# Kernel tuning notes

Measured on AMD Instinct MI355X. Metric: run time of the kernel, lower is better.

The kernel has to match this reference:

```python
import jax, jax.numpy as jnp
import numpy as np

N_USER = 100000
N_ITEM = 100000
E = 800000
IN_USER, IN_ITEM, HID, OUT = 256, 128, 128, 64


def _gconv(x_src, W, b, src, dst, n_src, n_dst):
    """DGL GraphConv, norm='both', transform-before-aggregate (in>=out here)."""
    ones = jnp.ones(src.shape[0], x_src.dtype)
    deg_out = jax.ops.segment_sum(ones, src, num_segments=n_src)
    deg_in = jax.ops.segment_sum(ones, dst, num_segments=n_dst)
    inv_out = jnp.maximum(deg_out, 1.0) ** -0.5
    inv_in = jnp.maximum(deg_in, 1.0) ** -0.5
    x = (x_src @ W) * inv_out[:, None]            # [n_src, out]
    agg = jax.ops.segment_sum(x[src], dst, num_segments=n_dst)  # scatter-add over edges
    return agg * inv_in[:, None] + b


def setup_inputs() -> dict:
    key = jax.random.key(0)
    ks = jax.random.split(key, 24)
    d = {
        "feat_user": jax.random.normal(ks[0], (N_USER, IN_USER), jnp.float32),
        "feat_item": jax.random.normal(ks[1], (N_ITEM, IN_ITEM), jnp.float32),
        "rates_src": jax.random.randint(ks[2], (E,), 0, N_USER, jnp.int32),
        "rates_dst": jax.random.randint(ks[3], (E,), 0, N_ITEM, jnp.int32),
        "rated_src": jax.random.randint(ks[4], (E,), 0, N_ITEM, jnp.int32),
        "rated_dst": jax.random.randint(ks[5], (E,), 0, N_USER, jnp.int32),
        "fol_src": jax.random.randint(ks[6], (E,), 0, N_USER, jnp.int32),
        "fol_dst": jax.random.randint(ks[7], (E,), 0, N_USER, jnp.int32),
    }
    def glorot(k, shp):
        lim = np.sqrt(6.0 / (shp[0] + shp[1]))
        return jax.random.uniform(k, shp, jnp.float32, -lim, lim)
    d["W1_rates"] = glorot(ks[8], (IN_USER, HID)); d["b1_rates"] = jnp.zeros((HID,), jnp.float32)
    d["W1_rated"] = glorot(ks[9], (IN_ITEM, HID)); d["b1_rated"] = jnp.zeros((HID,), jnp.float32)
    d["W1_fol"] = glorot(ks[10], (IN_USER, HID)); d["b1_fol"] = jnp.zeros((HID,), jnp.float32)
    d["W2_rates"] = glorot(ks[11], (HID, OUT)); d["b2_rates"] = jnp.zeros((OUT,), jnp.float32)
    d["W2_rated"] = glorot(ks[12], (HID, OUT)); d["b2_rated"] = jnp.zeros((OUT,), jnp.float32)
    d["W2_fol"] = glorot(ks[13], (HID, OUT)); d["b2_fol"] = jnp.zeros((OUT,), jnp.float32)
    return d


def reference(feat_user, feat_item, rates_src, rates_dst, rated_src, rated_dst,
              fol_src, fol_dst, W1_rates, b1_rates, W1_rated, b1_rated,
              W1_fol, b1_fol, W2_rates, b2_rates, W2_rated, b2_rated,
              W2_fol, b2_fol):
    # layer 1 (HeteroGraphConv, sum-aggregate across relations per dst ntype)
    h_item = _gconv(feat_user, W1_rates, b1_rates, rates_src, rates_dst, N_USER, N_ITEM)
    h_user = (_gconv(feat_item, W1_rated, b1_rated, rated_src, rated_dst, N_ITEM, N_USER)
              + _gconv(feat_user, W1_fol, b1_fol, fol_src, fol_dst, N_USER, N_USER))
    # relu (dropout = identity in eval mode)
    h_user = jax.nn.relu(h_user)
    h_item = jax.nn.relu(h_item)
    # layer 2
    o_item = _gconv(h_user, W2_rates, b2_rates, rates_src, rates_dst, N_USER, N_ITEM)
    o_user = (_gconv(h_item, W2_rated, b2_rated, rated_src, rated_dst, N_ITEM, N_USER)
              + _gconv(h_user, W2_fol, b2_fol, fol_src, fol_dst, N_USER, N_USER))
    return jnp.stack([o_user, o_item])  # [2, N, OUT]
```

## Files before the change

### kernel.cpp

```cpp
#include <hip/hip_runtime.h>
#include <math.h>

#define IN_USER 256
#define IN_ITEM 128
#define HID 128
#define OUTF 64
#define NRANGE 8
#define NCHUNK 16
#define MAXRB 12544

typedef unsigned short u16;
typedef unsigned int u32;
typedef __attribute__((ext_vector_type(8))) __bf16 bf16x8;
typedef __attribute__((ext_vector_type(4))) float f32x4;

__device__ __forceinline__ u16 f2bf(float f) {
    union { float f; u32 u; } c; c.f = f;
    return (u16)((c.u + 0x7fffu + ((c.u >> 16) & 1u)) >> 16);
}
__device__ __forceinline__ u32 pack2(float a, float b) {
    return (u32)f2bf(a) | ((u32)f2bf(b) << 16);
}

__global__ __launch_bounds__(512) void hist_ranges(
        const int* __restrict__ a0, int e0, const int* __restrict__ a1, int e1,
        const int* __restrict__ a2, int e2, const int* __restrict__ a3, int e3,
        const int* __restrict__ a4, int e4, const int* __restrict__ a5, int e5,
        int* __restrict__ hist, int NP, int RB) {
    __shared__ int h[MAXRB];
    const int a = blockIdx.z;
    const int* arr; int E;
    switch (a) {
        case 0: arr = a0; E = e0; break;
        case 1: arr = a1; E = e1; break;
        case 2: arr = a2; E = e2; break;
        case 3: arr = a3; E = e3; break;
        case 4: arr = a4; E = e4; break;
        default: arr = a5; E = e5; break;
    }
    const int c = blockIdx.y;
    const int lo = blockIdx.x * RB;
    const u32 rbu = (u32)RB;
    const int tid = threadIdx.x;
    for (int i = tid; i < RB; i += 512) h[i] = 0;
    __syncthreads();
    const int ec = (((E + NCHUNK - 1) / NCHUNK) + 3) & ~3;
    const int s0 = c * ec;
    const int s1 = (s0 + ec) < E ? (s0 + ec) : E;
    if (s1 > s0) {
        const int n4 = (s1 - s0) >> 2;
        const int4* p4 = reinterpret_cast<const int4*>(arr + s0);
        for (int i = tid; i < n4; i += 512) {
            const int4 A = p4[i];
            u32 ux = (u32)(A.x - lo); if (ux < rbu) atomicAdd(&h[ux], 1);
            u32 uy = (u32)(A.y - lo); if (uy < rbu) atomicAdd(&h[uy], 1);
            u32 uz = (u32)(A.z - lo); if (uz < rbu) atomicAdd(&h[uz], 1);
            u32 uw = (u32)(A.w - lo); if (uw < rbu) atomicAdd(&h[uw], 1);
        }
        for (int j = s0 + (n4 << 2) + tid; j < s1; j += 512) {
            const u32 u = (u32)(arr[j] - lo);
            if (u < rbu) atomicAdd(&h[u], 1);
        }
    }
    __syncthreads();
    int* out = hist + ((size_t)a * NCHUNK + c) * NP + lo;
    for (int i = tid; i < RB; i += 512) out[i] = h[i];
}

__global__ __launch_bounds__(256) void hist_reduce(
        int* __restrict__ hist, int* __restrict__ deg,
        float* __restrict__ inv, int NP) {
    const int a = blockIdx.y;
    const int v = blockIdx.x * 256 + threadIdx.x;
    if (v >= NP) return;
    int* h = hist + (size_t)a * NCHUNK * NP + v;
    int s = 0;
#pragma unroll
    for (int c = 0; c < NCHUNK; ++c) {
        const int t = h[(size_t)c * NP];
        if (a & 1) h[(size_t)c * NP] = s;
        s += t;
    }
    deg[(size_t)a * NP + v] = s;
    inv[(size_t)a * NP + v] = 1.0f / sqrtf((float)(s > 1 ? s : 1));
}

__global__ __launch_bounds__(256) void scan_part(
        const int* __restrict__ d0, const int* __restrict__ d1,
        const int* __restrict__ d2, int n0, int n1, int n2,
        int* __restrict__ partial, int nblk) {
    const int rel = blockIdx.y;
    const int* deg = rel == 0 ? d0 : (rel == 1 ? d1 : d2);
    const int n = rel == 0 ? n0 : (rel == 1 ? n1 : n2);
    const int base = blockIdx.x * 1024 + threadIdx.x * 4;
    int s = 0;
#pragma unroll
    for (int i = 0; i < 4; ++i) {
        const int idx = base + i;
        if (idx < n) s += deg[idx];
    }
    __shared__ int red[256];
    red[threadIdx.x] = s;
    __syncthreads();
#pragma unroll
    for (int off = 128; off > 0; off >>= 1) {
        if (threadIdx.x < off) red[threadIdx.x] += red[threadIdx.x + off];
        __syncthreads();
    }
    if (threadIdx.x == 0) partial[rel * nblk + blockIdx.x] = red[0];
}

__global__ __launch_bounds__(128) void scan_mid(int* __restrict__ partial, int nblk) {
    __shared__ int sc[128];
    const int rel = blockIdx.x;
    const int t = threadIdx.x;
    const int v = (t < nblk) ? partial[rel * nblk + t] : 0;
    sc[t] = v;
    __syncthreads();
    for (int off = 1; off < 128; off <<= 1) {
        const int u = (t >= off) ? sc[t - off] : 0;
        __syncthreads();
        sc[t] += u;
        __syncthreads();
    }
    if (t < nblk) partial[rel * nblk + t] = sc[t] - v;
}

__global__ __launch_bounds__(256) void scan_final(
        const int* __restrict__ d0, const int* __restrict__ d1,
        const int* __restrict__ d2, int n0, int n1, int n2,
        const int* __restrict__ partial,
        int* __restrict__ c0, int* __restrict__ c1, int* __restrict__ c2,
        int nblk) {
    const int rel = blockIdx.y;
    const int* deg = rel == 0 ? d0 : (rel == 1 ? d1 : d2);
    int* cur = rel == 0 ? c0 : (rel == 1 ? c1 : c2);
    const int n = rel == 0 ? n0 : (rel == 1 ? n1 : n2);
    const int base = blockIdx.x * 1024 + threadIdx.x * 4;
    int v[4];
    int s = 0;
#pragma unroll
    for (int i = 0; i < 4; ++i) {
        const int idx = base + i;
        v[i] = (idx < n) ? deg[idx] : 0;
        s += v[i];
    }
    __shared__ int sc[256];
    sc[threadIdx.x] = s;
    __syncthreads();
    for (int off = 1; off < 256; off <<= 1) {
        const int u = (threadIdx.x >= off) ? sc[threadIdx.x - off] : 0;
        __syncthreads();
        sc[threadIdx.x] += u;
        __syncthreads();
    }
    int run = (threadIdx.x == 0 ? 0 : sc[threadIdx.x - 1]) + partial[rel * nblk + blockIdx.x];
#pragma unroll
    for (int i = 0; i < 4; ++i) {
        const int idx = base + i;
        if (idx < n) cur[idx] = run;
        run += v[i];
    }
}

__global__ __launch_bounds__(512) void fill_ranges(
        const int* __restrict__ s0p, const int* __restrict__ d0p, int e0,
        const int* __restrict__ s1p, const int* __restrict__ d1p, int e1,
        const int* __restrict__ s2p, const int* __restrict__ d2p, int e2,
        const int* __restrict__ cursor, const int* __restrict__ hist,
        int NP, int RB,
        int* __restrict__ csrbase, int off1, int off2) {
    __shared__ int cur[MAXRB];
    const int rel = blockIdx.z;
    const int* src = rel == 0 ? s0p : (rel == 1 ? s1p : s2p);
    const int* dst = rel == 0 ? d0p : (rel == 1 ? d1p : d2p);
    const int E = rel == 0 ? e0 : (rel == 1 ? e1 : e2);
    int* csr = csrbase + (rel == 0 ? 0 : (rel == 1 ? off1 : off2));
    const int c = blockIdx.y;
    const int lo = blockIdx.x * RB;
    const u32 rbu = (u32)RB;
    const int tid = threadIdx.x;
    const int* gc = cursor + (size_t)rel * NP + lo;
    const int* go = hist + ((size_t)(2 * rel + 1) * NCHUNK + c) * NP + lo;
    for (int i = tid; i < RB; i += 512) cur[i] = gc[i] + go[i];
    __syncthreads();
    const int ec = (((E + NCHUNK - 1) / NCHUNK) + 3) & ~3;
    const int s0 = c * ec;
    const int s1 = (s0 + ec) < E ? (s0 + ec) : E;
    if (s1 > s0) {
        const int n4 = (s1 - s0) >> 2;
        const int4* d4 = reinterpret_cast<const int4*>(dst + s0);
        const int4* s4 = reinterpret_cast<const int4*>(src + s0);
        for (int i = tid; i < n4; i += 512) {
            const int4 D = d4[i], S = s4[i];
            u32 ux = (u32)(D.x - lo); if (ux < rbu) { int p = atomicAdd(&cur[ux], 1); csr[p] = S.x; }
            u32 uy = (u32)(D.y - lo); if (uy < rbu) { int p = atomicAdd(&cur[uy], 1); csr[p] = S.y; }
            u32 uz = (u32)(D.z - lo); if (uz < rbu) { int p = atomicAdd(&cur[uz], 1); csr[p] = S.z; }
            u32 uw = (u32)(D.w - lo); if (uw < rbu) { int p = atomicAdd(&cur[uw], 1); csr[p] = S.w; }
        }
        for (int j = s0 + (n4 << 2) + tid; j < s1; j += 512) {
            const u32 u = (u32)(dst[j] - lo);
            if (u < rbu) { const int p = atomicAdd(&cur[u], 1); csr[p] = src[j]; }
        }
    }
}

__global__ __launch_bounds__(256) void wt_all(
        u16* __restrict__ Wt1u, const float* __restrict__ W1_rates,
        const float* __restrict__ W1_fol,
        u16* __restrict__ Wt1i, const float* __restrict__ W1_rated,
        u16* __restrict__ Wt2u, const float* __restrict__ W2_rates,
        const float* __restrict__ W2_fol,
        u16* __restrict__ Wt2i, const float* __restrict__ W2_rated) {
    int i = blockIdx.x * 256 + threadIdx.x;
    if (i < 65536) {
        const int n = i >> 8, k = i & 255;
        const float v = (n < 128) ? W1_rates[k * 128 + n] : W1_fol[k * 128 + (n - 128)];
        Wt1u[(size_t)n * 256 + k] = f2bf(v);
        return;
    }
    i -= 65536;
    if (i < 16384) {
        const int n = i >> 7, k = i & 127;
        Wt1i[(size_t)n * 128 + k] = f2bf(W1_rated[k * 128 + n]);
        return;
    }
    i -= 16384;
    if (i < 16384) {
        const int n = i >> 7, k = i & 127;
        const float v = (n < 64) ? W2_rates[k * 64 + n] : W2_fol[k * 64 + (n - 64)];
        Wt2u[(size_t)n * 128 + k] = f2bf(v);
        return;
    }
    i -= 16384;
    if (i < 8192) {
        const int n = i >> 7, k = i & 127;
        Wt2i[(size_t)n * 128 + k] = f2bf(W2_rated[k * 64 + n]);
    }
}

template<int K, int BN, bool A_BF16>
__global__ __launch_bounds__(BN * 2) void gemm_mfma(
        const void* __restrict__ Xv, const u16* __restrict__ Wt,
        const float* __restrict__ invA, const float* __restrict__ invB,
        int nsplit, u16* __restrict__ T, int M, int TN) {
    constexpr int BLK = BN * 2;
    constexpr int WN = BN / 64;
    constexpr int CA = 1024 / BLK;
    constexpr int CB = (BN * 8) / BLK;
    __shared__ u16 lA[128 * 64];
    __shared__ u16 lB[BN * 64];

    const int tid = threadIdx.x;
    const int row0 = blockIdx.x * 128;
    const int col0 = blockIdx.y * BN;
    const int wid = tid >> 6, lane = tid & 63;
    const int wm = wid / WN, wn = wid % WN;
    const int l15 = lane & 15, lhi = lane >> 4;

    f32x4 acc[4][4] = {};

    for (int kk = 0; kk < K; kk += 64) {
        __syncthreads();
#pragma unroll
        for (int c = 0; c < CA; ++c) {
            const int cid = tid + c * BLK;
            const int row = cid >> 3, kc = cid & 7;
            const int grow = row0 + row;
            uint4 u = make_uint4(0, 0, 0, 0);
            if (A_BF16) {
                if (grow < M)
                    u = *reinterpret_cast<const uint4*>(
                        (const u16*)Xv + (size_t)grow * K + kk + kc * 8);
            } else {
                if (grow < M) {
                    const float* xp = (const float*)Xv + (size_t)grow * K + kk + kc * 8;
                    const float4 v0 = *reinterpret_cast<const float4*>(xp);
                    const float4 v1 = *reinterpret_cast<const float4*>(xp + 4);
                    u.x = pack2(v0.x, v0.y); u.y = pack2(v0.z, v0.w);
                    u.z = pack2(v1.x, v1.y); u.w = pack2(v1.z, v1.w);
                }
            }
            const int e = row * 64 + ((kc ^ (row & 7)) << 3);
            *reinterpret_cast<uint4*>(&lA[e]) = u;
        }
#pragma unroll
        for (int c = 0; c < CB; ++c) {
            const int cid = tid + c * BLK;
            const int n = cid >> 3, kc = cid & 7;
            const uint4 u = *reinterpret_cast<const uint4*>(
                Wt + (size_t)(col0 + n) * K + kk + kc * 8);
            const int e = n * 64 + ((kc ^ (n & 7)) << 3);
            *reinterpret_cast<uint4*>(&lB[e]) = u;
        }
        __syncthreads();
#pragma unroll
        for (int ks = 0; ks < 2; ++ks) {
            const int cb = ks * 4 + lhi;
            bf16x8 af[4], bfr[4];
#pragma unroll
            for (int fm = 0; fm < 4; ++fm) {
                const int r = wm * 64 + fm * 16 + l15;
                const uint4 u = *reinterpret_cast<const uint4*>(
                    &lA[r * 64 + ((cb ^ (r & 7)) << 3)]);
                af[fm] = __builtin_bit_cast(bf16x8, u);
            }
#pragma unroll
            for (int fn = 0; fn < 4; ++fn) {
                const int r = wn * 64 + fn * 16 + l15;
                const uint4 u = *reinterpret_cast<const uint4*>(
                    &lB[r * 64 + ((cb ^ (r & 7)) << 3)]);
                bfr[fn] = __builtin_bit_cast(bf16x8, u);
            }
#pragma unroll
            for (int fm = 0; fm < 4; ++fm)
#pragma unroll
                for (int fn = 0; fn < 4; ++fn)
                    acc[fm][fn] = __builtin_amdgcn_mfma_f32_16x16x32_bf16(
                        af[fm], bfr[fn], acc[fm][fn], 0, 0, 0);
        }
    }

    const int colw = col0 + wn * 64;
    const float* invp = (colw >= nsplit) ? invB : invA;
#pragma unroll
    for (int fm = 0; fm < 4; ++fm) {
#pragma unroll
        for (int r4 = 0; r4 < 4; ++r4) {
            const int grow = row0 + wm * 64 + fm * 16 + lhi * 4 + r4;
            if (grow < M) {
                const float s = invp[grow];
#pragma unroll
                for (int fn = 0; fn < 4; ++fn) {
                    const int col = colw + fn * 16 + l15;
                    T[(size_t)grow * TN + col] = f2bf(acc[fm][fn][r4] * s);
                }
            }
        }
    }
}

template<int F>
__device__ __forceinline__ void gather_rel(
        const u16* __restrict__ T, int strideT, int offT,
        const int* __restrict__ csr, int beg, int cnt, int Z, int lane,
        float& s0, float& s1) {
    const int* cp = csr + beg;
    const int loff = (F == 128) ? lane * 2 : lane;
    for (int e = 0; e < cnt; e += 8) {
        int idx[8];
#pragma unroll
        for (int i = 0; i < 8; ++i) {
            const int t = cp[e + i];
            idx[i] = __builtin_amdgcn_readfirstlane((e + i < cnt) ? t : Z);
        }
        if (F == 128) {
            u32 v[8];
#pragma unroll
            for (int i = 0; i < 8; ++i)
                v[i] = *reinterpret_cast<const u32*>(
                    T + (size_t)idx[i] * strideT + offT + loff);
#pragma unroll
            for (int i = 0; i < 8; ++i) {
                union { u32 u; float f; } lo, hi;
                lo.u = v[i] << 16;
                hi.u = v[i] & 0xffff0000u;
                s0 += lo.f; s1 += hi.f;
            }
        } else {
            u16 v[8];
#pragma unroll
            for (int i = 0; i < 8; ++i)
                v[i] = T[(size_t)idx[i] * strideT + offT + loff];
#pragma unroll
            for (int i = 0; i < 8; ++i) {
                union { u32 u; float f; } c;
                c.u = ((u32)v[i]) << 16;
                s0 += c.f;
            }
        }
    }
}

template<int F, bool TWO, bool RELU, bool BF16OUT>
__global__ __launch_bounds__(256) void gather(
        const u16* __restrict__ Ta, int strideA, int offA,
        const int* __restrict__ csrA, const int* __restrict__ curA,
        const int* __restrict__ degA, const float* __restrict__ invA,
        const float* __restrict__ biasA,
        const u16* __restrict__ Tb, int strideB, int offB,
        const int* __restrict__ csrB, const int* __restrict__ curB,
        const int* __restrict__ degB, const float* __restrict__ invB,
        const float* __restrict__ biasB,
        void* __restrict__ outv, int Z, int n) {
    const int wid = (blockIdx.x * 256 + threadIdx.x) >> 6;
    const int lane = threadIdx.x & 63;
    if (wid >= n) return;
    float r0, r1 = 0.f;
    {
        const int cnt = degA[wid];
        const int beg = curA[wid];
        float s0 = 0.f, s1 = 0.f;
        gather_rel<F>(Ta, strideA, offA, csrA, beg, cnt, Z, lane, s0, s1);
        const float a = invA[wid];
        if (F == 128) {
            const float2 b = *reinterpret_cast<const float2*>(biasA + lane * 2);
            r0 = s0 * a + b.x; r1 = s1 * a + b.y;
        } else {
            r0 = s0 * a + biasA[lane];
        }
    }
    if (TWO) {
        const int cnt = degB[wid];
        const int beg = curB[wid];
        float s0 = 0.f, s1 = 0.f;
        gather_rel<F>(Tb, strideB, offB, csrB, beg, cnt, Z, lane, s0, s1);
        const float a = invB[wid];
        if (F == 128) {
            const float2 b = *reinterpret_cast<const float2*>(biasB + lane * 2);
            r0 += s0 * a + b.x; r1 += s1 * a + b.y;
        } else {
            r0 += s0 * a + biasB[lane];
        }
    }
    if (RELU) { r0 = fmaxf(r0, 0.f); r1 = fmaxf(r1, 0.f); }
    if (BF16OUT) {
        if (F == 128)
            ((u32*)outv)[(size_t)wid * 64 + lane] = pack2(r0, r1);
        else
            ((u16*)outv)[(size_t)wid * 64 + lane] = f2bf(r0);
    } else {
        if (F == 128) {
            float2 o; o.x = r0; o.y = r1;
            *reinterpret_cast<float2*>((float*)outv + (size_t)wid * 128 + lane * 2) = o;
        } else {
            ((float*)outv)[(size_t)wid * 64 + lane] = r0;
        }
    }
}

extern "C" void kernel_launch(void* const* d_in, const int* in_sizes, int n_in,
                              void* d_out, int out_size, void* d_ws, size_t ws_size,
                              hipStream_t stream) {
    const float* feat_user = (const float*)d_in[0];
    const float* feat_item = (const float*)d_in[1];
    const int* rates_src = (const int*)d_in[2];
    const int* rates_dst = (const int*)d_in[3];
    const int* rated_src = (const int*)d_in[4];
    const int* rated_dst = (const int*)d_in[5];
    const int* fol_src   = (const int*)d_in[6];
    const int* fol_dst   = (const int*)d_in[7];
    const float* W1_rates = (const float*)d_in[8];
    const float* b1_rates = (const float*)d_in[9];
    const float* W1_rated = (const float*)d_in[10];
    const float* b1_rated = (const float*)d_in[11];
    const float* W1_fol   = (const float*)d_in[12];
    const float* b1_fol   = (const float*)d_in[13];
    const float* W2_rates = (const float*)d_in[14];
    const float* b2_rates = (const float*)d_in[15];
    const float* W2_rated = (const float*)d_in[16];
    const float* b2_rated = (const float*)d_in[17];
    const float* W2_fol   = (const float*)d_in[18];
    const float* b2_fol   = (const float*)d_in[19];

    const int n_user = in_sizes[0] / IN_USER;
    const int n_item = in_sizes[1] / IN_ITEM;
    const int E0 = in_sizes[2];
    const int E1 = in_sizes[4];
    const int E2 = in_sizes[6];
    const int nmax = n_user > n_item ? n_user : n_item;
    const int Z = nmax;

    const size_t NP = ((size_t)(nmax + 1023) / 1024) * 1024;
    int*   deg     = (int*)d_ws;
    float* inv     = (float*)(deg + 6 * NP);
    int*   cursor  = (int*)(inv + 6 * NP);
    int*   partial = cursor + 3 * NP;
    int*   csr  = partial + 3 * 128;
    int*   csr0 = csr;
    int*   csr1 = csr + E0;
    int*   csr2 = csr + E0 + E1;
    u16* Wt1u = (u16*)(csr + E0 + E1 + E2);
    u16* Wt1i = Wt1u + 256 * 256;
    u16* Wt2u = Wt1i + 128 * 128;
    u16* Wt2i = Wt2u + 128 * 128;
    u16* t1u  = Wt2i + 64 * 128;
    u16* t1i  = t1u + (size_t)(nmax + 1) * 256;
    u16* aggU = t1i + (size_t)(nmax + 1) * 128;
    u16* aggI = aggU + (size_t)nmax * 128;
    u16* t2u  = t1i;
    u16* t2i  = t1u;
    int* hist = (int*)t1u;

    float* o_user = (float*)d_out;
    float* o_item = o_user + (size_t)n_user * OUTF;

    hipMemsetAsync(t1u + (size_t)Z * 256, 0, 512, stream);
    hipMemsetAsync(t1i + (size_t)Z * 128, 0, 256, stream);

    const int RB = (int)(NP / NRANGE);
    hist_ranges<<<dim3(NRANGE, NCHUNK, 6), 512, 0, stream>>>(
        rates_src, E0, rates_dst, E0, rated_src, E1,
        rated_dst, E1, fol_src, E2, fol_dst, E2, hist, (int)NP, RB);
    hist_reduce<<<dim3((int)(NP + 255) / 256, 6), 256, 0, stream>>>(
        hist, deg, inv, (int)NP);

    wt_all<<<(65536 + 16384 + 16384 + 8192 + 255) / 256, 256, 0, stream>>>(
        Wt1u, W1_rates, W1_fol, Wt1i, W1_rated,
        Wt2u, W2_rates, W2_fol, Wt2i, W2_rated);

    const int nblk = (int)(NP / 1024);
    scan_part<<<dim3(nblk, 3), 256, 0, stream>>>(
        deg + 1 * NP, deg + 3 * NP, deg + 5 * NP, n_item, n_user, n_user, partial, nblk);
    scan_mid<<<3, 128, 0, stream>>>(partial, nblk);
    scan_final<<<dim3(nblk, 3), 256, 0, stream>>>(
        deg + 1 * NP, deg + 3 * NP, deg + 5 * NP, n_item, n_user, n_user, partial,
        cursor + 0 * NP, cursor + 1 * NP, cursor + 2 * NP, nblk);
    fill_ranges<<<dim3(NRANGE, NCHUNK, 3), 512, 0, stream>>>(
        rates_src, rates_dst, E0, rated_src, rated_dst, E1,
        fol_src, fol_dst, E2, cursor, hist, (int)NP, RB, csr, E0, E0 + E1);

    const int gbU = (n_user + 127) / 128;
    const int gbI = (n_item + 127) / 128;
    const int gwU = (n_user * 64 + 255) / 256;
    const int gwI = (n_item * 64 + 255) / 256;

    gemm_mfma<256, 128, false><<<dim3(gbU, 2), 256, 0, stream>>>(
        feat_user, Wt1u, inv + 0 * NP, inv + 4 * NP, 128, t1u, n_user, 256);
    gemm_mfma<128, 128, false><<<dim3(gbI, 1), 256, 0, stream>>>(
        feat_item, Wt1i, inv + 2 * NP, inv + 2 * NP, 1 << 30, t1i, n_item, 128);

    gather<128, false, true, true><<<gwI, 256, 0, stream>>>(
        t1u, 256, 0, csr0, cursor + 0 * NP, deg + 1 * NP, inv + 1 * NP, b1_rates,
        nullptr, 0, 0, nullptr, nullptr, nullptr, nullptr, nullptr,
        aggI, Z, n_item);
    gather<128, true, true, true><<<gwU, 256, 0, stream>>>(
        t1i, 128, 0, csr1, cursor + 1 * NP, deg + 3 * NP, inv + 3 * NP, b1_rated,
        t1u, 256, 128, csr2, cursor + 2 * NP, deg + 5 * NP, inv + 5 * NP, b1_fol,
        aggU, Z, n_user);

    hipMemsetAsync(t2i + (size_t)Z * 64, 0, 128, stream);

    gemm_mfma<128, 128, true><<<dim3(gbU, 1), 256, 0, stream>>>(
        aggU, Wt2u, inv + 0 * NP, inv + 4 * NP, 64, t2u, n_user, 128);
    gemm_mfma<128, 64, true><<<dim3(gbI, 1), 128, 0, stream>>>(
        aggI, Wt2i, inv + 2 * NP, inv + 2 * NP, 1 << 30, t2i, n_item, 64);

    gather<64, false, false, false><<<gwI, 256, 0, stream>>>(
        t2u, 128, 0, csr0, cursor + 0 * NP, deg + 1 * NP, inv + 1 * NP, b2_rates,
        nullptr, 0, 0, nullptr, nullptr, nullptr, nullptr, nullptr,
        o_item, Z, n_item);
    gather<64, true, false, false><<<gwU, 256, 0, stream>>>(
        t2i, 64, 0, csr1, cursor + 1 * NP, deg + 3 * NP, inv + 3 * NP, b2_rated,
        t2u, 128, 64, csr2, cursor + 2 * NP, deg + 5 * NP, inv + 5 * NP, b2_fol,
        o_user, Z, n_user);
}
```

Measured before the change: 449.2 us.

## Merge per-relation GEMM and gather launches into combined grid kernels

Pairs of independent GEMM launches and gather launches are merged into single kernels that dispatch on blockIdx.y, cutting the launch count and letting user and item work run concurrently instead of back to back. The GEMM is reworked so each block covers the full output width (BM×full N), with warp tiling chosen per case, which removes the y-split of the layer-1 user GEMM and rereads A only once. The cost is more shared memory per block (fixed at 20480 elements) and some idle blocks when the two halves have different grid sizes.

```diff
diff --git a/kernel.cpp b/kernel.cpp
--- a/kernel.cpp
+++ b/kernel.cpp
@@ -239,21 +239,20 @@
     }
 }
 
-template<int K, int BN, bool A_BF16>
-__global__ __launch_bounds__(BN * 2) void gemm_mfma(
+template<int WM, int WN, bool A_BF16>
+__device__ __forceinline__ void gemm_body(
+        u16* __restrict__ lbuf,
         const void* __restrict__ Xv, const u16* __restrict__ Wt,
         const float* __restrict__ invA, const float* __restrict__ invB,
-        int nsplit, u16* __restrict__ T, int M, int TN) {
-    constexpr int BLK = BN * 2;
-    constexpr int WN = BN / 64;
-    constexpr int CA = 1024 / BLK;
-    constexpr int CB = (BN * 8) / BLK;
-    __shared__ u16 lA[128 * 64];
-    __shared__ u16 lB[BN * 64];
-
+        int nsplit, u16* __restrict__ T, int M, int TN, int K, int bx) {
+    constexpr int BM = WM * 64, BN = WN * 64;
+    constexpr int BLK = WM * WN * 64;
+    constexpr int CA = 8 / WN;
+    constexpr int CB = 8 / WM;
+    u16* lA = lbuf;
+    u16* lB = lbuf + BM * 64;
     const int tid = threadIdx.x;
-    const int row0 = blockIdx.x * 128;
-    const int col0 = blockIdx.y * BN;
+    const int row0 = bx * BM;
     const int wid = tid >> 6, lane = tid & 63;
     const int wm = wid / WN, wn = wid % WN;
     const int l15 = lane & 15, lhi = lane >> 4;
@@ -281,17 +280,15 @@
                     u.z = pack2(v1.x, v1.y); u.w = pack2(v1.z, v1.w);
                 }
             }
-            const int e = row * 64 + ((kc ^ (row & 7)) << 3);
-            *reinterpret_cast<uint4*>(&lA[e]) = u;
+            *reinterpret_cast<uint4*>(&lA[row * 64 + ((kc ^ (row & 7)) << 3)]) = u;
         }
 #pragma unroll
         for (int c = 0; c < CB; ++c) {
             const int cid = tid + c * BLK;
             const int n = cid >> 3, kc = cid & 7;
             const uint4 u = *reinterpret_cast<const uint4*>(
-                Wt + (size_t)(col0 + n) * K + kk + kc * 8);
-            const int e = n * 64 + ((kc ^ (n & 7)) << 3);
-            *reinterpret_cast<uint4*>(&lB[e]) = u;
+                Wt + (size_t)n * K + kk + kc * 8);
+            *reinterpret_cast<uint4*>(&lB[n * 64 + ((kc ^ (n & 7)) << 3)]) = u;
         }
         __syncthreads();
 #pragma unroll
@@ -321,7 +318,7 @@
         }
     }
 
-    const int colw = col0 + wn * 64;
+    const int colw = wn * 64;
     const float* invp = (colw >= nsplit) ? invB : invA;
 #pragma unroll
     for (int fm = 0; fm < 4; ++fm) {
@@ -337,6 +334,38 @@
                 }
             }
         }
+    }
+}
+
+__global__ __launch_bounds__(256) void gemm_l1(
+        const float* __restrict__ Xu, const u16* __restrict__ Wt1u,
+        const float* __restrict__ Xi, const u16* __restrict__ Wt1i,
+        const float* __restrict__ inv0, const float* __restrict__ inv4,
+        const float* __restrict__ inv2,
+        u16* __restrict__ t1u, u16* __restrict__ t1i,
+        int nU, int nI, int gbI) {
+    __shared__ u16 lbuf[20480];
+    if (blockIdx.y == 0) {
+        gemm_body<1, 4, false>(lbuf, Xu, Wt1u, inv0, inv4, 128, t1u, nU, 256, 256, blockIdx.x);
+    } else {
+        if ((int)blockIdx.x >= gbI) return;
+        gemm_body<2, 2, false>(lbuf, Xi, Wt1i, inv2, inv2, 1 << 30, t1i, nI, 128, 128, blockIdx.x);
+    }
+}
+
+__global__ __launch_bounds__(256) void gemm_l2(
+        const u16* __restrict__ aggU, const u16* __restrict__ Wt2u,
+        const u16* __restrict__ aggI, const u16* __restrict__ Wt2i,
+        const float* __restrict__ inv0, const float* __restrict__ inv4,
+        const float* __restrict__ inv2,
+        u16* __restrict__ t2u, u16* __restrict__ t2i,
+        int nU, int nI, int gbI) {
+    __shared__ u16 lbuf[20480];
+    if (blockIdx.y == 0) {
+        gemm_body<2, 2, true>(lbuf, aggU, Wt2u, inv0, inv4, 64, t2u, nU, 128, 128, blockIdx.x);
+    } else {
+        if ((int)blockIdx.x >= gbI) return;
+        gemm_body<4, 1, true>(lbuf, aggI, Wt2i, inv2, inv2, 1 << 30, t2i, nI, 64, 128, blockIdx.x);
     }
 }
 
@@ -383,7 +412,7 @@
 }
 
 template<int F, bool TWO, bool RELU, bool BF16OUT>
-__global__ __launch_bounds__(256) void gather(
+__device__ __forceinline__ void gather_node(
         const u16* __restrict__ Ta, int strideA, int offA,
         const int* __restrict__ csrA, const int* __restrict__ curA,
         const int* __restrict__ degA, const float* __restrict__ invA,
@@ -392,10 +421,7 @@
         const int* __restrict__ csrB, const int* __restrict__ curB,
         const int* __restrict__ degB, const float* __restrict__ invB,
         const float* __restrict__ biasB,
-        void* __restrict__ outv, int Z, int n) {
-    const int wid = (blockIdx.x * 256 + threadIdx.x) >> 6;
-    const int lane = threadIdx.x & 63;
-    if (wid >= n) return;
+        void* __restrict__ outv, int Z, int wid, int lane) {
     float r0, r1 = 0.f;
     {
         const int cnt = degA[wid];
@@ -436,6 +462,66 @@
         } else {
             ((float*)outv)[(size_t)wid * 64 + lane] = r0;
         }
+    }
+}
+
+__global__ __launch_bounds__(256) void gather_l1(
+        const u16* __restrict__ t1u, const u16* __restrict__ t1i,
+        const int* __restrict__ csr0, const int* __restrict__ cur0,
+        const int* __restrict__ deg1, const float* __restrict__ inv1,
+        const float* __restrict__ b1_rates,
+        const int* __restrict__ csr1, const int* __restrict__ cur1,
+        const int* __restrict__ deg3, const float* __restrict__ inv3,
+        const float* __restrict__ b1_rated,
+        const int* __restrict__ csr2, const int* __restrict__ cur2,
+        const int* __restrict__ deg5, const float* __restrict__ inv5,
+        const float* __restrict__ b1_fol,
+        u16* __restrict__ aggI, u16* __restrict__ aggU,
+        int Z, int nI, int nU) {
+    const int wid = (blockIdx.x * 256 + threadIdx.x) >> 6;
+    const int lane = threadIdx.x & 63;
+    if (blockIdx.y == 0) {
+        if (wid >= nI) return;
+        gather_node<128, false, true, true>(
+            t1u, 256, 0, csr0, cur0, deg1, inv1, b1_rates,
+            nullptr, 0, 0, nullptr, nullptr, nullptr, nullptr, nullptr,
+            aggI, Z, wid, lane);
+    } else {
+        if (wid >= nU) return;
+        gather_node<128, true, true, true>(
+            t1i, 128, 0, csr1, cur1, deg3, inv3, b1_rated,
+            t1u, 256, 128, csr2, cur2, deg5, inv5, b1_fol,
+            aggU, Z, wid, lane);
+    }
+}
+
+__global__ __launch_bounds__(256) void gather_l2(
+        const u16* __restrict__ t2u, const u16* __restrict__ t2i,
+        const int* __restrict__ csr0, const int* __restrict__ cur0,
+        const int* __restrict__ deg1, const float* __restrict__ inv1,
+        const float* __restrict__ b2_rates,
+        const int* __restrict__ csr1, const int* __restrict__ cur1,
+        const int* __restrict__ deg3, const float* __restrict__ inv3,
+        const float* __restrict__ b2_rated,
+        const int* __restrict__ csr2, const int* __restrict__ cur2,
+        const int* __restrict__ deg5, const float* __restrict__ inv5,
+        const float* __restrict__ b2_fol,
+        float* __restrict__ o_item, float* __restrict__ o_user,
+        int Z, int nI, int nU) {
+    const int wid = (blockIdx.x * 256 + threadIdx.x) >> 6;
+    const int lane = threadIdx.x & 63;
+    if (blockIdx.y == 0) {
+        if (wid >= nI) return;
+        gather_node<64, false, false, false>(
+            t2u, 128, 0, csr0, cur0, deg1, inv1, b2_rates,
+            nullptr, 0, 0, nullptr, nullptr, nullptr, nullptr, nullptr,
+            o_item, Z, wid, lane);
+    } else {
+        if (wid >= nU) return;
+        gather_node<64, true, false, false>(
+            t2i, 64, 0, csr1, cur1, deg3, inv3, b2_rated,
+            t2u, 128, 64, csr2, cur2, deg5, inv5, b2_fol,
+            o_user, Z, wid, lane);
     }
 }
 
@@ -520,38 +606,35 @@
         rates_src, rates_dst, E0, rated_src, rated_dst, E1,
         fol_src, fol_dst, E2, cursor, hist, (int)NP, RB, csr, E0, E0 + E1);
 
-    const int gbU = (n_user + 127) / 128;
-    const int gbI = (n_item + 127) / 128;
-    const int gwU = (n_user * 64 + 255) / 256;
-    const int gwI = (n_item * 64 + 255) / 256;
-
-    gemm_mfma<256, 128, false><<<dim3(gbU, 2), 256, 0, stream>>>(
-        feat_user, Wt1u, inv + 0 * NP, inv + 4 * NP, 128, t1u, n_user, 256);
-    gemm_mfma<128, 128, false><<<dim3(gbI, 1), 256, 0, stream>>>(
-        feat_item, Wt1i, inv + 2 * NP, inv + 2 * NP, 1 << 30, t1i, n_item, 128);
-
-    gather<128, false, true, true><<<gwI, 256, 0, stream>>>(
-        t1u, 256, 0, csr0, cursor + 0 * NP, deg + 1 * NP, inv + 1 * NP, b1_rates,
-        nullptr, 0, 0, nullptr, nullptr, nullptr, nullptr, nullptr,
-        aggI, Z, n_item);
-    gather<128, true, true, true><<<gwU, 256, 0, stream>>>(
-        t1i, 128, 0, csr1, cursor + 1 * NP, deg + 3 * NP, inv + 3 * NP, b1_rated,
-        t1u, 256, 128, csr2, cursor + 2 * NP, deg + 5 * NP, inv + 5 * NP, b1_fol,
-        aggU, Z, n_user);
+    const int gbU1 = (n_user + 63) / 64;
+    const int gbI1 = (n_item + 127) / 128;
+    const int gbU2 = (n_user + 127) / 128;
+    const int gbI2 = (n_item + 255) / 256;
+    const int gw   = (nmax * 64 + 255) / 256;
+
+    gemm_l1<<<dim3(gbU1, 2), 256, 0, stream>>>(
+        feat_user, Wt1u, feat_item, Wt1i,
+        inv + 0 * NP, inv + 4 * NP, inv + 2 * NP,
+        t1u, t1i, n_user, n_item, gbI1);
+
+    gather_l1<<<dim3(gw, 2), 256, 0, stream>>>(
+        t1u, t1i,
+        csr0, cursor + 0 * NP, deg + 1 * NP, inv + 1 * NP, b1_rates,
+        csr1, cursor + 1 * NP, deg + 3 * NP, inv + 3 * NP, b1_rated,
+        csr2, cursor + 2 * NP, deg + 5 * NP, inv + 5 * NP, b1_fol,
+        aggI, aggU, Z, n_item, n_user);
 
     hipMemsetAsync(t2i + (size_t)Z * 64, 0, 128, stream);
 
-    gemm_mfma<128, 128, true><<<dim3(gbU, 1), 256, 0, stream>>>(
-        aggU, Wt2u, inv + 0 * NP, inv + 4 * NP, 64, t2u, n_user, 128);
-    gemm_mfma<128, 64, true><<<dim3(gbI, 1), 128, 0, stream>>>(
-        aggI, Wt2i, inv + 2 * NP, inv + 2 * NP, 1 << 30, t2i, n_item, 64);
-
-    gather<64, false, false, false><<<gwI, 256, 0, stream>>>(
-        t2u, 128, 0, csr0, cursor + 0 * NP, deg + 1 * NP, inv + 1 * NP, b2_rates,
-        nullptr, 0, 0, nullptr, nullptr, nullptr, nullptr, nullptr,
-        o_item, Z, n_item);
-    gather<64, true, false, false><<<gwU, 256, 0, stream>>>(
-        t2i, 64, 0, csr1, cursor + 1 * NP, deg + 3 * NP, inv + 3 * NP, b2_rated,
-        t2u, 128, 64, csr2, cursor + 2 * NP, deg + 5 * NP, inv + 5 * NP, b2_fol,
-        o_user, Z, n_user);
-}
+    gemm_l2<<<dim3(gbU2, 2), 256, 0, stream>>>(
+        aggU, Wt2u, aggI, Wt2i,
+        inv + 0 * NP, inv + 4 * NP, inv + 2 * NP,
+        t2u, t2i, n_user, n_item, gbI2);
+
+    gather_l2<<<dim3(gw, 2), 256, 0, stream>>>(
+        t2u, t2i,
+        csr0, cursor + 0 * NP, deg + 1 * NP, inv + 1 * NP, b2_rates,
+        csr1, cursor + 1 * NP, deg + 3 * NP, inv + 3 * NP, b2_rated,
+        csr2, cursor + 2 * NP, deg + 5 * NP, inv + 5 * NP, b2_fol,
+        o_item, o_user, Z, n_item, n_user);
+}
```

Measured after the change: 399.3 us, median of 2. 1.12x faster.
